# Optimization experiments

Measured on AMD Instinct MI355X. Metric: run time of the kernel, lower is better.

## Reference

```python
import jax, jax.numpy as jnp
import numpy as np

EPS = 1e-6      # flax LayerNorm default epsilon
DECAY = 0.1
LOG_ALPHA = 3.5


def _ln(x):
    # flax LayerNorm(reduction_axes=-2, use_bias=False, use_scale=False):
    # normalize over the token axis (-2), no affine params
    mu = x.mean(-2, keepdims=True)
    var = x.var(-2, keepdims=True)
    return (x - mu) * jax.lax.rsqrt(var + EPS)


def setup_inputs() -> dict:
    key = jax.random.key(0)
    ks = jax.random.split(key, 10)
    N, D, H, V = 4096, 64, 256, 8192
    xcat = jax.random.normal(ks[0], (N, D), jnp.float32)
    xsep = jnp.sort(jax.random.randint(ks[1], (N,), 0, 16)).astype(jnp.int32)
    xdiv = jax.random.randint(ks[2], (N,), 0, 2).astype(jnp.int32)
    esti = jax.random.normal(ks[3], (2, N, V), jnp.float32)
    output = jax.random.normal(ks[4], (D, V), jnp.float32) * 0.05
    # module params (init: normal(0.1) for delta/a/b, lecun_normal for Dense)
    delta = jax.random.normal(ks[5], (D, 1), jnp.float32) * 0.1
    a_p = jax.random.normal(ks[6], (D, 1), jnp.float32) * 0.1
    b_p = jax.random.normal(ks[7], (D, D), jnp.float32) * 0.1
    ffn_w1 = jax.random.normal(ks[8], (D, H), jnp.float32) * (1.0 / np.sqrt(D))
    ffn_b1 = jnp.zeros((H,), jnp.float32)
    ffn_w2 = jax.random.normal(ks[9], (H, D), jnp.float32) * (1.0 / np.sqrt(H))
    ffn_b2 = jnp.zeros((D,), jnp.float32)
    return dict(xcat=xcat, esti=esti, output=output, delta=delta, a_p=a_p,
                b_p=b_p, ffn_w1=ffn_w1, ffn_b1=ffn_b1, ffn_w2=ffn_w2,
                ffn_b2=ffn_b2, xsep=xsep, xdiv=xdiv, seed=0)


def reference(xcat, esti, output, delta, a_p, b_p, ffn_w1, ffn_b1, ffn_w2,
              ffn_b2, xsep, xdiv, seed):
    key = jax.random.key(seed)
    key, subkey = jax.random.split(key)
    # randomly drop dividers with prob DECAY
    xdiv = xdiv * (jax.random.uniform(subkey, xdiv.shape) > DECAY)
    t = jax.nn.log_sigmoid(xcat @ delta)  # [N,1] per-token "time"

    def op(x, y):
        xv, xt, xs, xd = x
        yv, yt, ys, yd = y
        dt = (yt - xt)[..., None]                         # [n,1,1]
        A = jnp.exp(dt * a_p) * b_p                       # [n,D,D] decay matrix
        m = ((xs == ys) & (xd == yd)).astype(xv.dtype)    # [n,1] segment mask
        return (yv + m * jnp.einsum('nd,nde->ne', xv, A), yt, ys, yd)

    div_id = xdiv.cumsum(0)[:, None]                      # [N,1]
    xnew, _, _, _ = jax.lax.associative_scan(
        op, (xcat, t, xsep[:, None], div_id), reverse=True, axis=0)

    # ffn = LN(axis=-2) -> Dense(H) -> relu -> Dense(D), residual with xcat
    h = _ln(xnew)
    h = jax.nn.relu(h @ ffn_w1 + ffn_b1) @ ffn_w2 + ffn_b2
    xnew = h + xcat

    xest = jax.nn.log_softmax(_ln(xnew) @ output, axis=-1)  # [N,V]
    gt = (esti[0].max(-1, keepdims=True) > LOG_ALPHA).astype(xest.dtype)  # [N,1]
    esti_new = jnp.stack([gt * esti[0] + (1 - gt) * xest,
                          gt * esti[1] + (1 - gt) * esti[0]], axis=0)
    return (xnew, esti_new)
```

## Files before the change

kernel.cpp:

```cpp
#include <hip/hip_runtime.h>
#include <stdint.h>

#define NN 4096
#define DD 64
#define HH 256
#define VV 8192
#define NVv ((size_t)NN*(size_t)VV)

typedef float f4 __attribute__((ext_vector_type(4)));
__device__ __forceinline__ f4 ntload(const f4* p){ return __builtin_nontemporal_load(p); }
__device__ __forceinline__ void ntstore(f4* p, f4 v){ __builtin_nontemporal_store(v, p); }

__device__ __forceinline__ uint32_t rotl32(uint32_t v, int r){ return (v<<r)|(v>>(32-r)); }
#define TF_ROUND(r) do { x0 += x1; x1 = rotl32(x1, r); x1 ^= x0; } while(0)
__device__ __forceinline__ void threefry2x32(uint32_t k0, uint32_t k1,
                                             uint32_t c0, uint32_t c1,
                                             uint32_t& o0, uint32_t& o1){
  uint32_t ks2 = k0 ^ k1 ^ 0x1BD11BDAu;
  uint32_t x0 = c0 + k0, x1 = c1 + k1;
  TF_ROUND(13); TF_ROUND(15); TF_ROUND(26); TF_ROUND(6);
  x0 += k1;  x1 += ks2 + 1u;
  TF_ROUND(17); TF_ROUND(29); TF_ROUND(16); TF_ROUND(24);
  x0 += ks2; x1 += k0 + 2u;
  TF_ROUND(13); TF_ROUND(15); TF_ROUND(26); TF_ROUND(6);
  x0 += k0;  x1 += k1 + 3u;
  TF_ROUND(17); TF_ROUND(29); TF_ROUND(16); TF_ROUND(24);
  x0 += k1;  x1 += ks2 + 4u;
  TF_ROUND(13); TF_ROUND(15); TF_ROUND(26); TF_ROUND(6);
  x0 += ks2; x1 += k0 + 5u;
  o0 = x0; o1 = x1;
}

__global__ __launch_bounds__(64) void k_t(const float* __restrict__ xcat,
                                          const float* __restrict__ delta,
                                          float* __restrict__ t){
  __shared__ float xr[64*65];
  __shared__ float dl[64];
  int b = blockIdx.x, tid = threadIdx.x;
  dl[tid] = delta[tid];
  const float4* src = (const float4*)(xcat + (size_t)b*4096);
  for (int i = tid; i < 1024; i += 64) {
    float4 v = src[i];
    int r = i >> 4, c = (i & 15)*4;
    float* p = &xr[r*65 + c];
    p[0]=v.x; p[1]=v.y; p[2]=v.z; p[3]=v.w;
  }
  __syncthreads();
  float acc = 0.f;
  #pragma unroll 16
  for (int d = 0; d < 64; ++d) acc = fmaf(xr[tid*65 + d], dl[d], acc);
  t[b*64 + tid] = fminf(acc, 0.f) - log1pf(expf(-fabsf(acc)));
}

__global__ __launch_bounds__(256) void k_rng(const int* __restrict__ xdiv,
                                             const int* __restrict__ seedp,
                                             int* __restrict__ dv){
  __shared__ int md[NN];
  __shared__ int ps[256];
  int tid = threadIdx.x;
  uint32_t seed = (uint32_t)seedp[0];
  uint32_t sk0, sk1;
  threefry2x32(0u, seed, 0u, 1u, sk0, sk1);
  for (int i = tid; i < NN; i += 256) {
    uint32_t o0, o1; threefry2x32(sk0, sk1, 0u, (uint32_t)i, o0, o1);
    uint32_t bits = o0 ^ o1;
    float u = __uint_as_float((bits>>9)|0x3f800000u) - 1.0f;
    md[i] = (u > 0.1f) ? xdiv[i] : 0;
  }
  __syncthreads();
  int base = tid*16, s = 0;
  #pragma unroll
  for (int k=0;k<16;k++){ s += md[base+k]; md[base+k] = s; }
  ps[tid] = s;
  __syncthreads();
  if (tid < 64) {
    int a0 = ps[4*tid], a1 = ps[4*tid+1], a2 = ps[4*tid+2], a3 = ps[4*tid+3];
    int s4 = a0+a1+a2+a3;
    int v = s4;
    #pragma unroll
    for (int o = 1; o < 64; o <<= 1) { int u = __shfl_up(v, o, 64); if (tid >= o) v += u; }
    int e = v - s4;
    ps[4*tid] = e; ps[4*tid+1] = e+a0; ps[4*tid+2] = e+a0+a1; ps[4*tid+3] = e+a0+a1+a2;
  }
  __syncthreads();
  int off = ps[tid];
  #pragma unroll
  for (int k=0;k<16;k++) dv[base+k] = md[base+k] + off;
}

__device__ __forceinline__ void wave_combine(const float* __restrict__ Xv,
                                             const float* __restrict__ Yv,
                                             float* __restrict__ Ov,
                                             int bidx, int cidx, int lane,
                                             const float* __restrict__ t,
                                             const int* __restrict__ sep,
                                             const int* __restrict__ dv,
                                             const float* __restrict__ al,
                                             const float* __restrict__ bl){
  int eb = (NN-1) - bidx, ec = (NN-1) - cidx;
  float acc = Yv[lane];
  if (sep[eb] == sep[ec] && dv[eb] == dv[ec]) {
    float dt = t[ec] - t[eb];
    float w = Xv[lane] * expf(dt * al[lane]);
    #pragma unroll 16
    for (int d = 0; d < 64; ++d)
      acc = fmaf(__shfl(w, d, 64), bl[d*64 + lane], acc);
  }
  Ov[lane] = acc;
}

__global__ __launch_bounds__(1024) void k_up(const float* __restrict__ xcat,
    const float* __restrict__ t, const int* __restrict__ sep, const int* __restrict__ dv,
    const float* __restrict__ ap, const float* __restrict__ bp, float* __restrict__ g7){
  __shared__ float G[255*64];
  __shared__ float bl[64*64];
  __shared__ float al[64];
  int b = blockIdx.x, tid = threadIdx.x, lane = tid & 63, wv = tid >> 6;
  for (int i = tid; i < 4096; i += 1024) bl[i] = bp[i];
  if (tid < 64) al[tid] = ap[tid];
  for (int k = wv; k < 128; k += 16) G[k*64 + lane] = xcat[(NN-1 - (128*b + k))*DD + lane];
  __syncthreads();
  const int Gof[8] = {0,128,192,224,240,248,252,254};
  for (int L = 1; L <= 7; ++L) {
    int nc = 128 >> L, s = 1 << (L-1);
    for (int c = wv; c < nc; c += 16)
      wave_combine(&G[(Gof[L-1]+2*c)*64], &G[(Gof[L-1]+2*c+1)*64], &G[(Gof[L]+c)*64],
                   128*b + (2*c+1)*s - 1, 128*b + (2*c+2)*s - 1, lane, t, sep, dv, al, bl);
    __syncthreads();
  }
  if (tid < 64) g7[b*64 + tid] = G[254*64 + tid];
}

__global__ __launch_bounds__(1024) void k_mid(const float* __restrict__ t,
    const int* __restrict__ sep, const int* __restrict__ dv,
    const float* __restrict__ ap, const float* __restrict__ bp,
    const float* __restrict__ g7, float* __restrict__ s7){
  __shared__ float G[63*64];
  __shared__ float R[63*64];
  __shared__ float bl[64*64];
  __shared__ float al[64];
  int tid = threadIdx.x, lane = tid & 63, wv = tid >> 6;
  for (int i = tid; i < 4096; i += 1024) bl[i] = bp[i];
  if (tid < 64) al[tid] = ap[tid];
  for (int k = wv; k < 32; k += 16) G[k*64 + lane] = g7[k*64 + lane];
  __syncthreads();
  const int Gof[13] = {0,0,0,0,0,0,0, 0,32,48,56,60,62};
  const int Rof[13] = {0,0,0,0,0,0,0, 31,15,7,3,1,0};
  for (int l = 8; l <= 12; ++l) {
    int nc = 1 << (12 - l), s = 1 << (l - 1);
    for (int c = wv; c < nc; c += 16)
      wave_combine(&G[(Gof[l-1]+2*c)*64], &G[(Gof[l-1]+2*c+1)*64], &G[(Gof[l]+c)*64],
                   (2*c+1)*s - 1, (2*c+2)*s - 1, lane, t, sep, dv, al, bl);
    __syncthreads();
  }
  if (tid < 64) R[Rof[12]*64 + tid] = G[Gof[12]*64 + tid];
  __syncthreads();
  for (int l = 11; l >= 7; --l) {
    int nL = 1 << (12 - l);
    for (int p = wv; p < nL; p += 16) {
      float* Ov = &R[(Rof[l]+p)*64];
      if (p == 0)        Ov[lane] = G[Gof[l]*64 + lane];
      else if (p & 1)    Ov[lane] = R[(Rof[l+1] + ((p-1)>>1))*64 + lane];
      else wave_combine(&R[(Rof[l+1] + (p>>1) - 1)*64], &G[(Gof[l]+p)*64], Ov,
                        p*(1<<l) - 1, (p+1)*(1<<l) - 1, lane, t, sep, dv, al, bl);
    }
    __syncthreads();
  }
  for (int k = wv; k < 32; k += 16) s7[k*64 + lane] = R[(31+k)*64 + lane];
}

__global__ __launch_bounds__(1024) void k_down(const float* __restrict__ xcat,
    const float* __restrict__ t, const int* __restrict__ sep, const int* __restrict__ dv,
    const float* __restrict__ ap, const float* __restrict__ bp,
    const float* __restrict__ s7, float* __restrict__ xs){
  __shared__ float G[254*64];
  __shared__ float R[255*64];
  __shared__ float bl[64*64];
  __shared__ float al[64];
  __shared__ float s7p[64];
  int b = blockIdx.x, tid = threadIdx.x, lane = tid & 63, wv = tid >> 6;
  for (int i = tid; i < 4096; i += 1024) bl[i] = bp[i];
  if (tid < 64) al[tid] = ap[tid];
  if (tid < 64) R[tid] = s7[b*64 + tid];
  if (tid >= 64 && tid < 128) s7p[tid-64] = (b > 0) ? s7[(b-1)*64 + (tid-64)] : 0.f;
  for (int k = wv; k < 128; k += 16) G[k*64 + lane] = xcat[(NN-1 - (128*b + k))*DD + lane];
  __syncthreads();
  const int Gof[7] = {0,128,192,224,240,248,252};
  const int Rof[8] = {127,63,31,15,7,3,1,0};
  for (int L = 1; L <= 6; ++L) {
    int nc = 128 >> L, s = 1 << (L-1);
    for (int c = wv; c < nc; c += 16)
      wave_combine(&G[(Gof[L-1]+2*c)*64], &G[(Gof[L-1]+2*c+1)*64], &G[(Gof[L]+c)*64],
                   128*b + (2*c+1)*s - 1, 128*b + (2*c+2)*s - 1, lane, t, sep, dv, al, bl);
    __syncthreads();
  }
  for (int L = 6; L >= 0; --L) {
    int nL = 1 << (7 - L);
    for (int p = wv; p < nL; p += 16) {
      float* Ov = &R[(Rof[L]+p)*64];
      int j = b*nL + p;
      if (j == 0)        Ov[lane] = G[Gof[L]*64 + lane];
      else if (p & 1)    Ov[lane] = R[(Rof[L+1] + ((p-1)>>1))*64 + lane];
      else {
        const float* Xv = (p == 0) ? s7p : &R[(Rof[L+1] + (p>>1) - 1)*64];
        wave_combine(Xv, &G[(Gof[L]+p)*64], Ov, j*(1<<L) - 1, (j+1)*(1<<L) - 1,
                     lane, t, sep, dv, al, bl);
      }
    }
    __syncthreads();
  }
  for (int p = wv; p < 128; p += 16)
    xs[(NN-1 - (128*b + p))*DD + lane] = R[(127+p)*64 + lane];
}

__global__ __launch_bounds__(256) void k_stats_part(const float* __restrict__ x,
                                                    float* __restrict__ part){
  __shared__ float s1[256], s2[256];
  int tid = threadIdx.x, d = tid & 63, r = tid >> 6, b = blockIdx.x;
  int n0 = b*16;
  float a = 0.f, q = 0.f;
  #pragma unroll
  for (int k = 0; k < 4; ++k) {
    float v = x[(n0 + r + 4*k)*DD + d];
    a += v; q = fmaf(v, v, q);
  }
  s1[tid] = a; s2[tid] = q;
  __syncthreads();
  if (tid < 64) {
    part[(b*2+0)*64 + tid] = s1[tid] + s1[tid+64] + s1[tid+128] + s1[tid+192];
    part[(b*2+1)*64 + tid] = s2[tid] + s2[tid+64] + s2[tid+128] + s2[tid+192];
  }
}

__global__ __launch_bounds__(256) void k_stats_fin(const float* __restrict__ part,
                                                   float* __restrict__ mu,
                                                   float* __restrict__ rs){
  __shared__ float s1[256], s2[256];
  int tid = threadIdx.x, d = tid & 63, p = tid >> 6;
  float a = 0.f, q = 0.f;
  #pragma unroll 8
  for (int i = p; i < 256; i += 4) {
    a += part[(i*2+0)*64 + d];
    q += part[(i*2+1)*64 + d];
  }
  s1[tid] = a; s2[tid] = q;
  __syncthreads();
  if (tid < 64) {
    float S = s1[tid]+s1[tid+64]+s1[tid+128]+s1[tid+192];
    float Q = s2[tid]+s2[tid+64]+s2[tid+128]+s2[tid+192];
    float m = S/(float)NN;
    float var = fmaxf(Q/(float)NN - m*m, 0.f);
    mu[tid] = m; rs[tid] = rsqrtf(var + 1e-6f);
  }
}

__global__ __launch_bounds__(256) void k_ffn(const float* __restrict__ xs,
    const float* __restrict__ xcat, const float* __restrict__ mu, const float* __restrict__ rs,
    const float* __restrict__ w1, const float* __restrict__ b1,
    const float* __restrict__ w2, const float* __restrict__ b2,
    float* __restrict__ xnew){
  __shared__ float xln[16*64];
  __shared__ float Hl[16*HH];
  int b = blockIdx.x, tid = threadIdx.x;
  int n0 = b*16;
  for (int idx = tid; idx < 1024; idx += 256) {
    int i = idx >> 6, d = idx & 63;
    xln[idx] = (xs[(n0+i)*DD + d] - mu[d]) * rs[d];
  }
  float w1c[64];
  #pragma unroll
  for (int d = 0; d < 64; ++d) w1c[d] = w1[d*HH + tid];
  float bb1 = b1[tid];
  __syncthreads();
  #pragma unroll 2
  for (int i = 0; i < 16; ++i) {
    float acc = bb1;
    #pragma unroll
    for (int d = 0; d < 64; ++d) acc = fmaf(xln[i*64 + d], w1c[d], acc);
    Hl[i*HH + tid] = fmaxf(acc, 0.f);
  }
  __syncthreads();
  int e = tid & 63, ig = tid >> 6;
  for (int k = 0; k < 4; ++k) {
    int i = ig + 4*k;
    float acc = b2[e];
    #pragma unroll 8
    for (int h = 0; h < HH; ++h) acc = fmaf(Hl[i*HH + h], w2[h*DD + e], acc);
    int n = n0 + i;
    xnew[n*DD + e] = acc + xcat[n*DD + e];
  }
}

#define FMA4(Z,W) do { Z.x=fmaf(xv,W.x,Z.x); Z.y=fmaf(xv,W.y,Z.y); \
                       Z.z=fmaf(xv,W.z,Z.z); Z.w=fmaf(xv,W.w,Z.w); } while(0)
#define MAX4(M,V) M = fmaxf(M, fmaxf(fmaxf(V.x,V.y), fmaxf(V.z,V.w)))
__global__ __launch_bounds__(256)
__attribute__((amdgpu_waves_per_eu(2, 4)))
void k_est(const float* __restrict__ xnew,
    const float* __restrict__ mu, const float* __restrict__ rs,
    const float* __restrict__ outw, const float* __restrict__ esti,
    float* __restrict__ dout){
  __shared__ float xl[64];
  __shared__ float r4a[4], r4b[4], r4c[4];
  int n = blockIdx.x, tid = threadIdx.x, lane = tid & 63, wv = tid >> 6;
  const f4* e0 = (const f4*)(esti + (size_t)n*VV);
  const f4* e1 = (const f4*)(esti + NVv + (size_t)n*VV);
  f4* o0 = (f4*)(dout + (size_t)NN*DD + (size_t)n*VV);
  f4* o1 = (f4*)(dout + (size_t)NN*DD + NVv + (size_t)n*VV);
  if (tid < 64) xl[tid] = (xnew[n*DD + tid] - mu[tid]) * rs[tid];
  f4 a0 = ntload(e0+tid),      a1 = ntload(e0+tid+256),
     a2 = ntload(e0+tid+512),  a3 = ntload(e0+tid+768),
     a4 = ntload(e0+tid+1024), a5 = ntload(e0+tid+1280),
     a6 = ntload(e0+tid+1536), a7 = ntload(e0+tid+1792);
  float mx = -1e30f;
  MAX4(mx,a0); MAX4(mx,a1); MAX4(mx,a2); MAX4(mx,a3);
  MAX4(mx,a4); MAX4(mx,a5); MAX4(mx,a6); MAX4(mx,a7);
  #pragma unroll
  for (int o = 32; o; o >>= 1) mx = fmaxf(mx, __shfl_xor(mx, o, 64));
  if (lane == 0) r4a[wv] = mx;
  __syncthreads();
  float m0 = fmaxf(fmaxf(r4a[0], r4a[1]), fmaxf(r4a[2], r4a[3]));
  if (m0 > 3.5f) {
    ntstore(o0+tid,      a0); ntstore(o0+tid+256,  a1);
    ntstore(o0+tid+512,  a2); ntstore(o0+tid+768,  a3);
    ntstore(o0+tid+1024, a4); ntstore(o0+tid+1280, a5);
    ntstore(o0+tid+1536, a6); ntstore(o0+tid+1792, a7);
    f4 b0 = ntload(e1+tid),      b1 = ntload(e1+tid+256),
       b2 = ntload(e1+tid+512),  b3 = ntload(e1+tid+768),
       b4 = ntload(e1+tid+1024), b5 = ntload(e1+tid+1280),
       b6 = ntload(e1+tid+1536), b7 = ntload(e1+tid+1792);
    ntstore(o1+tid,      b0); ntstore(o1+tid+256,  b1);
    ntstore(o1+tid+512,  b2); ntstore(o1+tid+768,  b3);
    ntstore(o1+tid+1024, b4); ntstore(o1+tid+1280, b5);
    ntstore(o1+tid+1536, b6); ntstore(o1+tid+1792, b7);
    return;
  }
  ntstore(o1+tid,      a0); ntstore(o1+tid+256,  a1);
  ntstore(o1+tid+512,  a2); ntstore(o1+tid+768,  a3);
  ntstore(o1+tid+1024, a4); ntstore(o1+tid+1280, a5);
  ntstore(o1+tid+1536, a6); ntstore(o1+tid+1792, a7);
  f4 z00 = {0,0,0,0}, z01 = {0,0,0,0}, z02 = {0,0,0,0}, z03 = {0,0,0,0};
  for (int d = 0; d < 64; ++d) {
    float xv = xl[d];
    const f4* wr = (const f4*)(outw + (size_t)d*VV) + tid;
    f4 w0 = wr[0], w1 = wr[256], w2 = wr[512], w3 = wr[768];
    FMA4(z00,w0); FMA4(z01,w1); FMA4(z02,w2); FMA4(z03,w3);
  }
  f4 z10 = {0,0,0,0}, z11 = {0,0,0,0}, z12 = {0,0,0,0}, z13 = {0,0,0,0};
  for (int d = 0; d < 64; ++d) {
    float xv = xl[d];
    const f4* wr = (const f4*)(outw + (size_t)d*VV) + tid + 1024;
    f4 w0 = wr[0], w1 = wr[256], w2 = wr[512], w3 = wr[768];
    FMA4(z10,w0); FMA4(z11,w1); FMA4(z12,w2); FMA4(z13,w3);
  }
  float zmax = -1e30f;
  MAX4(zmax,z00); MAX4(zmax,z01); MAX4(zmax,z02); MAX4(zmax,z03);
  MAX4(zmax,z10); MAX4(zmax,z11); MAX4(zmax,z12); MAX4(zmax,z13);
  #pragma unroll
  for (int o = 32; o; o >>= 1) zmax = fmaxf(zmax, __shfl_xor(zmax, o, 64));
  if (lane == 0) r4b[wv] = zmax;
  __syncthreads();
  zmax = fmaxf(fmaxf(r4b[0], r4b[1]), fmaxf(r4b[2], r4b[3]));
  float s = 0.f;
  #define SUM4(V) s += expf(V.x - zmax) + expf(V.y - zmax) + expf(V.z - zmax) + expf(V.w - zmax)
  SUM4(z00); SUM4(z01); SUM4(z02); SUM4(z03);
  SUM4(z10); SUM4(z11); SUM4(z12); SUM4(z13);
  #undef SUM4
  #pragma unroll
  for (int o = 32; o; o >>= 1) s += __shfl_xor(s, o, 64);
  if (lane == 0) r4c[wv] = s;
  __syncthreads();
  float lse = zmax + logf(r4c[0] + r4c[1] + r4c[2] + r4c[3]);
  #define STO(Z,OFF) do { f4 v=Z; v.x-=lse; v.y-=lse; v.z-=lse; v.w-=lse; ntstore(o0+(OFF), v); } while(0)
  STO(z00, tid);        STO(z01, tid + 256);  STO(z02, tid + 512);  STO(z03, tid + 768);
  STO(z10, tid + 1024); STO(z11, tid + 1280); STO(z12, tid + 1536); STO(z13, tid + 1792);
  #undef STO
}

extern "C" void kernel_launch(void* const* d_in, const int* in_sizes, int n_in,
                              void* d_out, int out_size, void* d_ws, size_t ws_size,
                              hipStream_t stream) {
  const float* xcat = (const float*)d_in[0];
  const float* esti = (const float*)d_in[1];
  const float* outw = (const float*)d_in[2];
  const float* delta= (const float*)d_in[3];
  const float* ap   = (const float*)d_in[4];
  const float* bp   = (const float*)d_in[5];
  const float* w1   = (const float*)d_in[6];
  const float* b1   = (const float*)d_in[7];
  const float* w2   = (const float*)d_in[8];
  const float* b2   = (const float*)d_in[9];
  const int* xsep   = (const int*)d_in[10];
  const int* xdiv   = (const int*)d_in[11];
  const int* seedp  = (const int*)d_in[12];
  float* out = (float*)d_out;

  char* ws = (char*)d_ws;
  float* t    = (float*)(ws);
  int*   dv   = (int*)  (ws + 16384);
  float* g7   = (float*)(ws + 32768);
  float* s7   = (float*)(ws + 40960);
  float* xs   = (float*)(ws + 49152);
  float* mu1  = (float*)(ws + 49152 + 1048576);
  float* rs1  = mu1 + 64;
  float* mu2  = rs1 + 64;
  float* rs2  = mu2 + 64;
  float* part = (float*)(ws + 49152 + 1048576 + 4096);

  hipLaunchKernelGGL(k_t,          dim3(64),   dim3(64),   0, stream, xcat, delta, t);
  hipLaunchKernelGGL(k_rng,        dim3(1),    dim3(256),  0, stream, xdiv, seedp, dv);
  hipLaunchKernelGGL(k_up,         dim3(32),   dim3(1024), 0, stream, xcat, t, xsep, dv, ap, bp, g7);
  hipLaunchKernelGGL(k_mid,        dim3(1),    dim3(1024), 0, stream, t, xsep, dv, ap, bp, g7, s7);
  hipLaunchKernelGGL(k_down,       dim3(32),   dim3(1024), 0, stream, xcat, t, xsep, dv, ap, bp, s7, xs);
  hipLaunchKernelGGL(k_stats_part, dim3(256),  dim3(256),  0, stream, xs, part);
  hipLaunchKernelGGL(k_stats_fin,  dim3(1),    dim3(256),  0, stream, part, mu1, rs1);
  hipLaunchKernelGGL(k_ffn,        dim3(256),  dim3(256),  0, stream, xs, xcat, mu1, rs1, w1, b1, w2, b2, out);
  hipLaunchKernelGGL(k_stats_part, dim3(256),  dim3(256),  0, stream, out, part);
  hipLaunchKernelGGL(k_stats_fin,  dim3(1),    dim3(256),  0, stream, part, mu2, rs2);
  hipLaunchKernelGGL(k_est,        dim3(NN),   dim3(256),  0, stream, out, mu2, rs2, outw, esti, out);
}
```

Measured before the change: 268.5 us.

## Merge small kernels and fuse LayerNorm stats into the FFN kernel

Merges the per-token time kernel and the RNG/cumsum kernel into one launch, with block 64 doing the RNG work. Each FFN block now redundantly finalizes the first LayerNorm stats from the partial sums, and its epilogue emits partial sums for the second LayerNorm. This drops three launches and one full pass over the output. The cost is redundant stats reduction in every FFN block and extra shared memory.

```diff
diff --git a/kernel.cpp b/kernel.cpp
--- a/kernel.cpp
+++ b/kernel.cpp
@@ -31,33 +31,36 @@
   o0 = x0; o1 = x1;
 }
 
-__global__ __launch_bounds__(64) void k_t(const float* __restrict__ xcat,
-                                          const float* __restrict__ delta,
-                                          float* __restrict__ t){
+__global__ __launch_bounds__(256) void k_pre(const float* __restrict__ xcat,
+                                             const float* __restrict__ delta,
+                                             const int* __restrict__ xdiv,
+                                             const int* __restrict__ seedp,
+                                             float* __restrict__ t,
+                                             int* __restrict__ dv){
   __shared__ float xr[64*65];
   __shared__ float dl[64];
-  int b = blockIdx.x, tid = threadIdx.x;
-  dl[tid] = delta[tid];
-  const float4* src = (const float4*)(xcat + (size_t)b*4096);
-  for (int i = tid; i < 1024; i += 64) {
-    float4 v = src[i];
-    int r = i >> 4, c = (i & 15)*4;
-    float* p = &xr[r*65 + c];
-    p[0]=v.x; p[1]=v.y; p[2]=v.z; p[3]=v.w;
-  }
-  __syncthreads();
-  float acc = 0.f;
-  #pragma unroll 16
-  for (int d = 0; d < 64; ++d) acc = fmaf(xr[tid*65 + d], dl[d], acc);
-  t[b*64 + tid] = fminf(acc, 0.f) - log1pf(expf(-fabsf(acc)));
-}
-
-__global__ __launch_bounds__(256) void k_rng(const int* __restrict__ xdiv,
-                                             const int* __restrict__ seedp,
-                                             int* __restrict__ dv){
-  __shared__ int md[NN];
-  __shared__ int ps[256];
+  __shared__ int   md[NN];
+  __shared__ int   ps[256];
   int tid = threadIdx.x;
+  if (blockIdx.x < 64) {
+    int b = blockIdx.x;
+    if (tid < 64) dl[tid] = delta[tid];
+    const float4* src = (const float4*)(xcat + (size_t)b*4096);
+    for (int i = tid; i < 1024; i += 256) {
+      float4 v = src[i];
+      int r = i >> 4, c = (i & 15)*4;
+      float* p = &xr[r*65 + c];
+      p[0]=v.x; p[1]=v.y; p[2]=v.z; p[3]=v.w;
+    }
+    __syncthreads();
+    if (tid < 64) {
+      float acc = 0.f;
+      #pragma unroll 16
+      for (int d = 0; d < 64; ++d) acc = fmaf(xr[tid*65 + d], dl[d], acc);
+      t[b*64 + tid] = fminf(acc, 0.f) - log1pf(expf(-fabsf(acc)));
+    }
+    return;
+  }
   uint32_t seed = (uint32_t)seedp[0];
   uint32_t sk0, sk1;
   threefry2x32(0u, seed, 0u, 1u, sk0, sk1);
@@ -255,17 +258,38 @@
 }
 
 __global__ __launch_bounds__(256) void k_ffn(const float* __restrict__ xs,
-    const float* __restrict__ xcat, const float* __restrict__ mu, const float* __restrict__ rs,
+    const float* __restrict__ xcat, const float* __restrict__ part1,
     const float* __restrict__ w1, const float* __restrict__ b1,
     const float* __restrict__ w2, const float* __restrict__ b2,
-    float* __restrict__ xnew){
+    float* __restrict__ xnew, float* __restrict__ part2){
   __shared__ float xln[16*64];
   __shared__ float Hl[16*HH];
+  __shared__ float s1[256], s2[256];
+  __shared__ float mu_s[64], rs_s[64];
   int b = blockIdx.x, tid = threadIdx.x;
   int n0 = b*16;
+  {
+    int d = tid & 63, p = tid >> 6;
+    float a = 0.f, q = 0.f;
+    #pragma unroll 8
+    for (int i = p; i < 256; i += 4) {
+      a += part1[(i*2+0)*64 + d];
+      q += part1[(i*2+1)*64 + d];
+    }
+    s1[tid] = a; s2[tid] = q;
+    __syncthreads();
+    if (tid < 64) {
+      float S = s1[tid]+s1[tid+64]+s1[tid+128]+s1[tid+192];
+      float Q = s2[tid]+s2[tid+64]+s2[tid+128]+s2[tid+192];
+      float m = S/(float)NN;
+      float var = fmaxf(Q/(float)NN - m*m, 0.f);
+      mu_s[tid] = m; rs_s[tid] = rsqrtf(var + 1e-6f);
+    }
+    __syncthreads();
+  }
   for (int idx = tid; idx < 1024; idx += 256) {
     int i = idx >> 6, d = idx & 63;
-    xln[idx] = (xs[(n0+i)*DD + d] - mu[d]) * rs[d];
+    xln[idx] = (xs[(n0+i)*DD + d] - mu_s[d]) * rs_s[d];
   }
   float w1c[64];
   #pragma unroll
@@ -281,13 +305,22 @@
   }
   __syncthreads();
   int e = tid & 63, ig = tid >> 6;
+  float a2 = 0.f, q2 = 0.f;
   for (int k = 0; k < 4; ++k) {
     int i = ig + 4*k;
     float acc = b2[e];
     #pragma unroll 8
     for (int h = 0; h < HH; ++h) acc = fmaf(Hl[i*HH + h], w2[h*DD + e], acc);
     int n = n0 + i;
-    xnew[n*DD + e] = acc + xcat[n*DD + e];
+    float v = acc + xcat[n*DD + e];
+    xnew[n*DD + e] = v;
+    a2 += v; q2 = fmaf(v, v, q2);
+  }
+  s1[tid] = a2; s2[tid] = q2;
+  __syncthreads();
+  if (tid < 64) {
+    part2[(b*2+0)*64 + tid] = s1[tid] + s1[tid+64] + s1[tid+128] + s1[tid+192];
+    part2[(b*2+1)*64 + tid] = s2[tid] + s2[tid+64] + s2[tid+128] + s2[tid+192];
   }
 }
 
@@ -396,26 +429,22 @@
   float* out = (float*)d_out;
 
   char* ws = (char*)d_ws;
-  float* t    = (float*)(ws);
-  int*   dv   = (int*)  (ws + 16384);
-  float* g7   = (float*)(ws + 32768);
-  float* s7   = (float*)(ws + 40960);
-  float* xs   = (float*)(ws + 49152);
-  float* mu1  = (float*)(ws + 49152 + 1048576);
-  float* rs1  = mu1 + 64;
-  float* mu2  = rs1 + 64;
-  float* rs2  = mu2 + 64;
-  float* part = (float*)(ws + 49152 + 1048576 + 4096);
-
-  hipLaunchKernelGGL(k_t,          dim3(64),   dim3(64),   0, stream, xcat, delta, t);
-  hipLaunchKernelGGL(k_rng,        dim3(1),    dim3(256),  0, stream, xdiv, seedp, dv);
+  float* t     = (float*)(ws);
+  int*   dv    = (int*)  (ws + 16384);
+  float* g7    = (float*)(ws + 32768);
+  float* s7    = (float*)(ws + 40960);
+  float* xs    = (float*)(ws + 49152);
+  float* mu2   = (float*)(ws + 49152 + 1048576);
+  float* rs2   = mu2 + 64;
+  float* part1 = (float*)(ws + 49152 + 1048576 + 4096);
+  float* part2 = (float*)(ws + 49152 + 1048576 + 4096 + 131072);
+
+  hipLaunchKernelGGL(k_pre,        dim3(65),   dim3(256),  0, stream, xcat, delta, xdiv, seedp, t, dv);
   hipLaunchKernelGGL(k_up,         dim3(32),   dim3(1024), 0, stream, xcat, t, xsep, dv, ap, bp, g7);
   hipLaunchKernelGGL(k_mid,        dim3(1),    dim3(1024), 0, stream, t, xsep, dv, ap, bp, g7, s7);
   hipLaunchKernelGGL(k_down,       dim3(32),   dim3(1024), 0, stream, xcat, t, xsep, dv, ap, bp, s7, xs);
-  hipLaunchKernelGGL(k_stats_part, dim3(256),  dim3(256),  0, stream, xs, part);
-  hipLaunchKernelGGL(k_stats_fin,  dim3(1),    dim3(256),  0, stream, part, mu1, rs1);
-  hipLaunchKernelGGL(k_ffn,        dim3(256),  dim3(256),  0, stream, xs, xcat, mu1, rs1, w1, b1, w2, b2, out);
-  hipLaunchKernelGGL(k_stats_part, dim3(256),  dim3(256),  0, stream, out, part);
-  hipLaunchKernelGGL(k_stats_fin,  dim3(1),    dim3(256),  0, stream, part, mu2, rs2);
+  hipLaunchKernelGGL(k_stats_part, dim3(256),  dim3(256),  0, stream, xs, part1);
+  hipLaunchKernelGGL(k_ffn,        dim3(256),  dim3(256),  0, stream, xs, xcat, part1, w1, b1, w2, b2, out, part2);
+  hipLaunchKernelGGL(k_stats_fin,  dim3(1),    dim3(256),  0, stream, part2, mu2, rs2);
   hipLaunchKernelGGL(k_est,        dim3(NN),   dim3(256),  0, stream, out, mu2, rs2, outw, esti, out);
 }
```

New measurement: 262.3 us. 1.02x faster.
